# Kernel tuning notes

Hardware: AMD Instinct MI355X
Metric: run time of the kernel (lower is better)

## Reference

```python
import jax, jax.numpy as jnp
import numpy as np
import math

P = 7          # patch / kernel size (must be odd for onion-peeling: N = 1+4*m*(m+1) = P*P)
EPS = 1e-6
EPS_W = 0.5

def _ball_dirs():
    u = [np.array([[1.0, 0.0]])]
    s = [np.zeros(1)]
    for k in range(1, P // 2 + 1):
        n = 8 * k
        th = np.linspace(0.0, 2.0 * math.pi * (1.0 - 1.0 / n), n)
        u.append(np.stack([np.cos(th), np.sin(th)], 1))
        s.append(np.full(n, k / (P // 2)))
    return (np.concatenate(u, 0).astype(np.float32), np.concatenate(s).astype(np.float32))

_U, _S = _ball_dirs()  # [N,2], [N], N == P*P == 49

def _forward(x, metric_w, metric_b, proj_w, proj_b):
    B, C, H, W = x.shape
    Hp, Wp = H // P, W // P
    u = jnp.asarray(_U)
    s = jnp.asarray(_S)
    # metric net: strided conv -> 7 params per patch
    params = jax.lax.conv_general_dilated(
        x, metric_w, (P, P), 'VALID',
        dimension_numbers=('NCHW', 'OIHW', 'NCHW')) + metric_b[None, :, None, None]
    v_raw = jnp.moveaxis(params[:, :2], 1, -1)                      # [B,Hp,Wp,2]
    v = v_raw / jnp.maximum(jnp.linalg.norm(v_raw, axis=-1, keepdims=True), 1e-12)
    eig = 2.0 * jax.nn.sigmoid(jnp.moveaxis(params[:, 2:4], 1, -1))  # [B,Hp,Wp,2]
    scale = 0.5 + 1.5 * jax.nn.sigmoid(jnp.moveaxis(params[:, 4:5], 1, -1))
    eig = eig * scale
    vp = jnp.stack([-v[..., 1], v[..., 0]], -1)
    R = jnp.stack([v, vp], -1)                                      # [B,Hp,Wp,2,2] (columns v, v_perp)
    M = R @ (eig[..., None] * jnp.swapaxes(R, -1, -2))              # R diag(eig) R^T
    w = params[:, 5:7]                                              # [B,2,Hp,Wp]
    w = w * (1.0 - EPS_W) * jax.nn.sigmoid(jnp.linalg.norm(w, axis=1, keepdims=True))
    # Finsler-Randers norm F(u) = sqrt(u^T M u + eps) + w.u for all N unit dirs
    quad = jnp.einsum('nj,bhwij,ni->bnhw', u, M, u)                 # [B,N,Hp,Wp]
    drift = jnp.einsum('bihw,ni->bnhw', w, u)
    F_u = jnp.sqrt(quad + EPS) + drift
    y = (u[None, :, :, None, None] / (F_u[:, :, None] + EPS)
         * s[None, :, None, None, None])                            # [B,N,2,Hp,Wp]
    y = y.reshape(B, P, P, 2, Hp, Wp)[:, :, :, ::-1]                # flip last coord pair (x,y)->(y,x)
    gi = jnp.arange(P, dtype=x.dtype) - P // 2
    grid = jnp.stack(jnp.meshgrid(gi, gi, indexing='ij'), -1)       # [P,P,2]
    off = y - grid[None, :, :, :, None, None]                       # [B,P,P,2,Hp,Wp]
    off_y = jnp.transpose(off[:, :, :, 0], (0, 3, 4, 1, 2))         # [B,Hp,Wp,P,P]
    off_x = jnp.transpose(off[:, :, :, 1], (0, 3, 4, 1, 2))
    base_h = (jnp.arange(Hp, dtype=x.dtype) * P)[None, :, None, None, None]
    base_w = (jnp.arange(Wp, dtype=x.dtype) * P)[None, None, :, None, None]
    ki = jnp.arange(P, dtype=x.dtype)
    py = off_y + base_h + ki[None, None, None, :, None]             # sample rows
    px = off_x + base_w + ki[None, None, None, None, :]             # sample cols
    # bilinear sampling with zero padding (torchvision deform_conv2d semantics)
    y0 = jnp.floor(py)
    x0 = jnp.floor(px)
    wy = py - y0
    wx = px - x0

    def gather(yi, xi):
        valid = (yi >= 0) & (yi <= H - 1) & (xi >= 0) & (xi <= W - 1)
        yc = jnp.clip(yi, 0, H - 1).astype(jnp.int32)
        xc = jnp.clip(xi, 0, W - 1).astype(jnp.int32)
        vals = jax.vmap(lambda img, yy, xx: img[:, yy, xx])(x, yc, xc)  # [B,C,Hp,Wp,P,P]
        return vals * valid[:, None].astype(x.dtype)

    sampled = (gather(y0, x0) * ((1 - wy) * (1 - wx))[:, None]
               + gather(y0, x0 + 1) * ((1 - wy) * wx)[:, None]
               + gather(y0 + 1, x0) * (wy * (1 - wx))[:, None]
               + gather(y0 + 1, x0 + 1) * (wy * wx)[:, None])       # [B,C,Hp,Wp,P,P]
    out = jnp.einsum('bchwij,ecij->behw', sampled, proj_w) + proj_b[None, :, None, None]
    return jnp.moveaxis(out.reshape(B, out.shape[1], -1), 1, 2)     # [B, Hp*Wp, E]

def setup_inputs():
    key = jax.random.key(0)
    k0, k1, k2 = jax.random.split(key, 3)
    B, C, H, W, E = 64, 3, 224, 224, 384
    x = jax.random.normal(k0, (B, C, H, W), jnp.float32)
    metric_w = jax.random.normal(k1, (7, C, P, P), jnp.float32) / math.sqrt(C * P * P)
    metric_b = jnp.zeros((7,), jnp.float32)
    proj_w = jax.random.normal(k2, (E, C, P, P), jnp.float32) / (P * math.sqrt(C))
    proj_b = jnp.zeros((E,), jnp.float32)
    return {"x": x, "metric_w": metric_w, "metric_b": metric_b,
            "proj_w": proj_w, "proj_b": proj_b}

def reference(x, metric_w, metric_b, proj_w, proj_b):
    return _forward(x, metric_w, metric_b, proj_w, proj_b)
```

## Files before the change

kernel.cpp:

```cpp
#include <hip/hip_runtime.h>
#include <math.h>

#define PP   7
#define NDIR 49
#define CIN  3
#define KK   147
#define KPAD 160
#define EE   384
#define HH   224
#define WW   224
#define GG   16
#define TB   256
#define SSTR 17
#define NPX  112

typedef __attribute__((ext_vector_type(8))) __bf16 bf16x8;
typedef __attribute__((ext_vector_type(4))) float  f32x4;

__device__ __forceinline__ float sigmoidf_(float v) {
    return 1.0f / (1.0f + expf(-v));
}

__global__ void pack_pw_kernel(const float* __restrict__ pw, unsigned short* __restrict__ pwB) {
    int idx = blockIdx.x * blockDim.x + threadIdx.x;
    if (idx < EE * KPAD) {
        int e = idx / KPAD;
        int k = idx - e * KPAD;
        float v = (k < KK) ? pw[e * KK + k] : 0.0f;
        __bf16 h = (__bf16)v;
        pwB[idx] = *(unsigned short*)&h;
    }
}

__global__ void pack_x_kernel(const float* __restrict__ x, float* __restrict__ xp, int npix) {
    int idx = blockIdx.x * blockDim.x + threadIdx.x;
    if (idx >= npix) return;
    int b = idx / (HH * WW);
    int p = idx - b * (HH * WW);
    const float* xb = x + (size_t)b * (CIN * HH * WW) + p;
    f32x4 v;
    v[0] = xb[0];
    v[1] = xb[HH * WW];
    v[2] = xb[2 * HH * WW];
    v[3] = 0.0f;
    *(f32x4*)(xp + (size_t)idx * 4) = v;
}

template<bool PACKED>
__launch_bounds__(TB)
__global__ void fused_kernel(const float* __restrict__ x,
                             const float* __restrict__ xp,
                             const float* __restrict__ mw,
                             const float* __restrict__ mb,
                             const unsigned short* __restrict__ pwB,
                             const float* __restrict__ pb,
                             float* __restrict__ out) {
    __shared__ float mws[7 * KK];
    __shared__ float dirs[NDIR][3];
    __shared__ float par_s[GG][8];
    __shared__ float der_s[GG][5];
    __shared__ float buf[3136];

    const int t   = threadIdx.x;
    const int blk = blockIdx.x;
    const int b   = blk >> 6;
    const int rem = blk & 63;
    const int hp  = rem >> 1;
    const int wp0 = (rem & 1) * GG;
    const size_t m0 = (size_t)blk * GG;
    const int row0 = hp * PP;
    const int col0 = wp0 * PP;

    for (int i = t; i < 7 * KK; i += TB) mws[i] = mw[i];
    if (t >= 64 && t < 64 + NDIR) {
        int n = t - 64;
        float u0, u1, s;
        if (n == 0)      { u0 = 1.0f; u1 = 0.0f; s = 0.0f; }
        else if (n < 9)  { float th = (float)(n - 1)  * 0.78539816339744831f; u0 = cosf(th); u1 = sinf(th); s = 0.33333334f; }
        else if (n < 25) { float th = (float)(n - 9)  * 0.39269908169872414f; u0 = cosf(th); u1 = sinf(th); s = 0.66666669f; }
        else             { float th = (float)(n - 25) * 0.26179938779914941f; u0 = cosf(th); u1 = sinf(th); s = 1.0f; }
        dirs[n][0] = u0; dirs[n][1] = u1; dirs[n][2] = s;
    }

    if (PACKED) {
        for (int item = t; item < 7 * NPX; item += TB) {
            int i = item / NPX, px = item - i * NPX;
            f32x4 v = *(const f32x4*)(xp + ((size_t)((b * HH + row0 + i) * WW) + col0 + px) * 4);
            *(f32x4*)&buf[item * 4] = v;
        }
    } else {
        for (int item = t; item < CIN * 7 * NPX; item += TB) {
            int c = item / (7 * NPX), r2 = item - c * (7 * NPX);
            int i = r2 / NPX, px = r2 - i * NPX;
            buf[item] = x[(size_t)b * (CIN * HH * WW) + (size_t)c * (HH * WW)
                          + (size_t)(row0 + i) * WW + col0 + px];
        }
    }
    __syncthreads();

    if (t < 112) {
        int prm = t >> 4, g = t & 15;
        float acc = mb[prm];
        const float* wrow = &mws[prm * KK];
        #pragma unroll
        for (int c = 0; c < CIN; ++c) {
            #pragma unroll
            for (int i = 0; i < 7; ++i) {
                #pragma unroll
                for (int j = 0; j < 7; ++j) {
                    float xv = PACKED ? buf[(i * NPX + g * 7 + j) * 4 + c]
                                      : buf[(c * 7 + i) * NPX + g * 7 + j];
                    acc = fmaf(xv, wrow[c * 49 + i * 7 + j], acc);
                }
            }
        }
        par_s[g][prm] = acc;
    }
    __syncthreads();

    if (t < GG) {
        float a0 = par_s[t][0], a1 = par_s[t][1], a2 = par_s[t][2], a3 = par_s[t][3];
        float a4 = par_s[t][4], a5 = par_s[t][5], a6 = par_s[t][6];
        float nrm = sqrtf(a0 * a0 + a1 * a1);
        float inv = 1.0f / fmaxf(nrm, 1e-12f);
        float v0 = a0 * inv, v1 = a1 * inv;
        float e0 = 2.0f * sigmoidf_(a2);
        float e1 = 2.0f * sigmoidf_(a3);
        float sc = 0.5f + 1.5f * sigmoidf_(a4);
        e0 *= sc; e1 *= sc;
        float wn  = sqrtf(a5 * a5 + a6 * a6);
        float wsc = 0.5f * sigmoidf_(wn);
        der_s[t][0] = e0 * v0 * v0 + e1 * v1 * v1;
        der_s[t][1] = (e0 - e1) * v0 * v1;
        der_s[t][2] = e0 * v1 * v1 + e1 * v0 * v0;
        der_s[t][3] = a5 * wsc;
        der_s[t][4] = a6 * wsc;
    }
    __syncthreads();

    const float* xb = x + (size_t)b * (CIN * HH * WW);
    const size_t pbase = (size_t)b * (HH * WW);
    for (int item = t; item < GG * NDIR; item += TB) {
        int g = item / NDIR;
        int n = item - g * NDIR;
        float u0 = dirs[n][0], u1 = dirs[n][1], s = dirs[n][2];
        float M00 = der_s[g][0], M01 = der_s[g][1], M11 = der_s[g][2];
        float w0 = der_s[g][3], w1 = der_s[g][4];
        float quad  = u0 * u0 * M00 + 2.0f * u0 * u1 * M01 + u1 * u1 * M11;
        float drift = w0 * u0 + w1 * u1;
        float F = sqrtf(quad + 1e-6f) + drift;
        float r = s / (F + 1e-6f);
        float py = (float)(row0 + 3) + u1 * r;
        float px = (float)(col0 + g * PP + 3) + u0 * r;
        float y0f = floorf(py), x0f = floorf(px);
        float y1f = y0f + 1.0f, x1f = x0f + 1.0f;
        float wy = py - y0f, wx = px - x0f;
        bool vy0 = (y0f >= 0.0f) && (y0f <= (float)(HH - 1));
        bool vy1 = (y1f >= 0.0f) && (y1f <= (float)(HH - 1));
        bool vx0 = (x0f >= 0.0f) && (x0f <= (float)(WW - 1));
        bool vx1 = (x1f >= 0.0f) && (x1f <= (float)(WW - 1));
        int iy0 = (int)fminf(fmaxf(y0f, 0.0f), (float)(HH - 1));
        int iy1 = (int)fminf(fmaxf(y1f, 0.0f), (float)(HH - 1));
        int ix0 = (int)fminf(fmaxf(x0f, 0.0f), (float)(WW - 1));
        int ix1 = (int)fminf(fmaxf(x1f, 0.0f), (float)(WW - 1));
        float w00 = (1.0f - wy) * (1.0f - wx);
        float w01 = (1.0f - wy) * wx;
        float w10 = wy * (1.0f - wx);
        float w11 = wy * wx;
        if (PACKED) {
            float c00 = w00 * ((vy0 && vx0) ? 1.0f : 0.0f);
            float c01 = w01 * ((vy0 && vx1) ? 1.0f : 0.0f);
            float c10 = w10 * ((vy1 && vx0) ? 1.0f : 0.0f);
            float c11 = w11 * ((vy1 && vx1) ? 1.0f : 0.0f);
            f32x4 q00 = *(const f32x4*)(xp + (pbase + (size_t)(iy0 * WW + ix0)) * 4);
            f32x4 q01 = *(const f32x4*)(xp + (pbase + (size_t)(iy0 * WW + ix1)) * 4);
            f32x4 q10 = *(const f32x4*)(xp + (pbase + (size_t)(iy1 * WW + ix0)) * 4);
            f32x4 q11 = *(const f32x4*)(xp + (pbase + (size_t)(iy1 * WW + ix1)) * 4);
            #pragma unroll
            for (int c = 0; c < CIN; ++c) {
                buf[(c * NDIR + n) * SSTR + g] =
                    q00[c] * c00 + q01[c] * c01 + q10[c] * c10 + q11[c] * c11;
            }
        } else {
            #pragma unroll
            for (int c = 0; c < CIN; ++c) {
                const float* xc = xb + c * (HH * WW);
                float v00 = (vy0 && vx0) ? xc[iy0 * WW + ix0] : 0.0f;
                float v01 = (vy0 && vx1) ? xc[iy0 * WW + ix1] : 0.0f;
                float v10 = (vy1 && vx0) ? xc[iy1 * WW + ix0] : 0.0f;
                float v11 = (vy1 && vx1) ? xc[iy1 * WW + ix1] : 0.0f;
                buf[(c * NDIR + n) * SSTR + g] =
                    v00 * w00 + v01 * w01 + v10 * w10 + v11 * w11;
            }
        }
    }
    __syncthreads();

    const int lane = t & 63;
    const int wv   = t >> 6;
    const int nrow = lane & 15;
    const int hi   = lane >> 4;

    bf16x8 afr[5];
    #pragma unroll
    for (int ks = 0; ks < 5; ++ks) {
        #pragma unroll
        for (int j = 0; j < 8; ++j) {
            int k = ks * 32 + hi * 8 + j;
            float v = (k < KK) ? buf[k * SSTR + nrow] : 0.0f;
            afr[ks][j] = (__bf16)v;
        }
    }

    #pragma unroll
    for (int q = 0; q < 6; ++q) {
        int tile = wv * 6 + q;
        int e    = tile * 16 + nrow;
        const unsigned short* brow = pwB + (size_t)e * KPAD + hi * 8;
        f32x4 acc = {0.0f, 0.0f, 0.0f, 0.0f};
        #pragma unroll
        for (int ks = 0; ks < 5; ++ks) {
            bf16x8 bfr = *(const bf16x8*)&brow[ks * 32];
            acc = __builtin_amdgcn_mfma_f32_16x16x32_bf16(afr[ks], bfr, acc, 0, 0, 0);
        }
        float bias = pb[e];
        #pragma unroll
        for (int r = 0; r < 4; ++r) {
            out[(m0 + hi * 4 + r) * EE + e] = acc[r] + bias;
        }
    }
}

extern "C" void kernel_launch(void* const* d_in, const int* in_sizes, int n_in,
                              void* d_out, int out_size, void* d_ws, size_t ws_size,
                              hipStream_t stream) {
    const float* x  = (const float*)d_in[0];
    const float* mw = (const float*)d_in[1];
    const float* mb = (const float*)d_in[2];
    const float* pw = (const float*)d_in[3];
    const float* pb = (const float*)d_in[4];
    float* out = (float*)d_out;

    unsigned short* pwB = (unsigned short*)d_ws;
    float* xp = (float*)((char*)d_ws + (size_t)(1 << 17));

    const int B = in_sizes[0] / (CIN * HH * WW);
    const int npix = B * HH * WW;
    const size_t need = (size_t)(1 << 17) + (size_t)npix * 4 * sizeof(float);
    const bool packed = ws_size >= need;

    pack_pw_kernel<<<(EE * KPAD + 255) / 256, 256, 0, stream>>>(pw, pwB);
    if (packed) {
        pack_x_kernel<<<(npix + 255) / 256, 256, 0, stream>>>(x, xp, npix);
        fused_kernel<true><<<B * 64, TB, 0, stream>>>(x, xp, mw, mb, pwB, pb, out);
    } else {
        fused_kernel<false><<<B * 64, TB, 0, stream>>>(x, xp, mw, mb, pwB, pb, out);
    }
}
```

Baseline: 235.7 us.

## Drop packed-x pre-pass, gather from planar input, transpose MFMA for vector stores

Removes the pack_x pre-kernel and its interleaved RGBA workspace, so every block reads the planar input directly for both the metric conv tile and the bilinear gather. This cuts the shared buffer size and adds a launch bound of 6 blocks per CU for occupancy. The gather now loads unconditionally from clamped indices and masks the weights instead of the loads. The MFMA operands are swapped so each lane holds four consecutive output channels, allowing float4 bias loads and float4 output stores. The risk is less coalesced gather traffic on the planar layout, which now takes three scalar loads per corner instead of one vector load.

```diff
diff --git a/kernel.cpp b/kernel.cpp
--- a/kernel.cpp
+++ b/kernel.cpp
@@ -32,24 +32,8 @@
     }
 }
 
-__global__ void pack_x_kernel(const float* __restrict__ x, float* __restrict__ xp, int npix) {
-    int idx = blockIdx.x * blockDim.x + threadIdx.x;
-    if (idx >= npix) return;
-    int b = idx / (HH * WW);
-    int p = idx - b * (HH * WW);
-    const float* xb = x + (size_t)b * (CIN * HH * WW) + p;
-    f32x4 v;
-    v[0] = xb[0];
-    v[1] = xb[HH * WW];
-    v[2] = xb[2 * HH * WW];
-    v[3] = 0.0f;
-    *(f32x4*)(xp + (size_t)idx * 4) = v;
-}
-
-template<bool PACKED>
-__launch_bounds__(TB)
+__launch_bounds__(TB, 6)
 __global__ void fused_kernel(const float* __restrict__ x,
-                             const float* __restrict__ xp,
                              const float* __restrict__ mw,
                              const float* __restrict__ mb,
                              const unsigned short* __restrict__ pwB,
@@ -59,7 +43,7 @@
     __shared__ float dirs[NDIR][3];
     __shared__ float par_s[GG][8];
     __shared__ float der_s[GG][5];
-    __shared__ float buf[3136];
+    __shared__ __align__(16) float buf[2512];
 
     const int t   = threadIdx.x;
     const int blk = blockIdx.x;
@@ -71,6 +55,8 @@
     const int row0 = hp * PP;
     const int col0 = wp0 * PP;
 
+    const float* xb = x + (size_t)b * (CIN * HH * WW);
+
     for (int i = t; i < 7 * KK; i += TB) mws[i] = mw[i];
     if (t >= 64 && t < 64 + NDIR) {
         int n = t - 64;
@@ -82,39 +68,33 @@
         dirs[n][0] = u0; dirs[n][1] = u1; dirs[n][2] = s;
     }
 
-    if (PACKED) {
-        for (int item = t; item < 7 * NPX; item += TB) {
-            int i = item / NPX, px = item - i * NPX;
-            f32x4 v = *(const f32x4*)(xp + ((size_t)((b * HH + row0 + i) * WW) + col0 + px) * 4);
-            *(f32x4*)&buf[item * 4] = v;
-        }
-    } else {
-        for (int item = t; item < CIN * 7 * NPX; item += TB) {
-            int c = item / (7 * NPX), r2 = item - c * (7 * NPX);
-            int i = r2 / NPX, px = r2 - i * NPX;
-            buf[item] = x[(size_t)b * (CIN * HH * WW) + (size_t)c * (HH * WW)
-                          + (size_t)(row0 + i) * WW + col0 + px];
-        }
+    for (int item = t; item < CIN * 7 * NPX; item += TB) {
+        int c = item / (7 * NPX), r2 = item - c * (7 * NPX);
+        int i = r2 / NPX, px = r2 - i * NPX;
+        buf[item] = xb[(size_t)c * (HH * WW) + (size_t)(row0 + i) * WW + col0 + px];
     }
     __syncthreads();
 
     if (t < 112) {
         int prm = t >> 4, g = t & 15;
-        float acc = mb[prm];
         const float* wrow = &mws[prm * KK];
-        #pragma unroll
-        for (int c = 0; c < CIN; ++c) {
+        float acc0 = 0.0f, acc1 = 0.0f, acc2 = 0.0f;
+        #pragma unroll 1
+        for (int i = 0; i < 7; ++i) {
+            const float* b0 = &buf[(0 * 7 + i) * NPX + g * 7];
+            const float* b1 = &buf[(1 * 7 + i) * NPX + g * 7];
+            const float* b2 = &buf[(2 * 7 + i) * NPX + g * 7];
+            const float* w0 = &wrow[i * 7];
+            const float* w1 = &wrow[49 + i * 7];
+            const float* w2 = &wrow[98 + i * 7];
             #pragma unroll
-            for (int i = 0; i < 7; ++i) {
-                #pragma unroll
-                for (int j = 0; j < 7; ++j) {
-                    float xv = PACKED ? buf[(i * NPX + g * 7 + j) * 4 + c]
-                                      : buf[(c * 7 + i) * NPX + g * 7 + j];
-                    acc = fmaf(xv, wrow[c * 49 + i * 7 + j], acc);
-                }
+            for (int j = 0; j < 7; ++j) {
+                acc0 = fmaf(b0[j], w0[j], acc0);
+                acc1 = fmaf(b1[j], w1[j], acc1);
+                acc2 = fmaf(b2[j], w2[j], acc2);
             }
         }
-        par_s[g][prm] = acc;
+        par_s[g][prm] = mb[prm] + acc0 + acc1 + acc2;
     }
     __syncthreads();
 
@@ -138,59 +118,48 @@
     }
     __syncthreads();
 
-    const float* xb = x + (size_t)b * (CIN * HH * WW);
-    const size_t pbase = (size_t)b * (HH * WW);
-    for (int item = t; item < GG * NDIR; item += TB) {
-        int g = item / NDIR;
-        int n = item - g * NDIR;
-        float u0 = dirs[n][0], u1 = dirs[n][1], s = dirs[n][2];
-        float M00 = der_s[g][0], M01 = der_s[g][1], M11 = der_s[g][2];
-        float w0 = der_s[g][3], w1 = der_s[g][4];
-        float quad  = u0 * u0 * M00 + 2.0f * u0 * u1 * M01 + u1 * u1 * M11;
-        float drift = w0 * u0 + w1 * u1;
-        float F = sqrtf(quad + 1e-6f) + drift;
-        float r = s / (F + 1e-6f);
-        float py = (float)(row0 + 3) + u1 * r;
-        float px = (float)(col0 + g * PP + 3) + u0 * r;
-        float y0f = floorf(py), x0f = floorf(px);
-        float y1f = y0f + 1.0f, x1f = x0f + 1.0f;
-        float wy = py - y0f, wx = px - x0f;
-        bool vy0 = (y0f >= 0.0f) && (y0f <= (float)(HH - 1));
-        bool vy1 = (y1f >= 0.0f) && (y1f <= (float)(HH - 1));
-        bool vx0 = (x0f >= 0.0f) && (x0f <= (float)(WW - 1));
-        bool vx1 = (x1f >= 0.0f) && (x1f <= (float)(WW - 1));
-        int iy0 = (int)fminf(fmaxf(y0f, 0.0f), (float)(HH - 1));
-        int iy1 = (int)fminf(fmaxf(y1f, 0.0f), (float)(HH - 1));
-        int ix0 = (int)fminf(fmaxf(x0f, 0.0f), (float)(WW - 1));
-        int ix1 = (int)fminf(fmaxf(x1f, 0.0f), (float)(WW - 1));
-        float w00 = (1.0f - wy) * (1.0f - wx);
-        float w01 = (1.0f - wy) * wx;
-        float w10 = wy * (1.0f - wx);
-        float w11 = wy * wx;
-        if (PACKED) {
-            float c00 = w00 * ((vy0 && vx0) ? 1.0f : 0.0f);
-            float c01 = w01 * ((vy0 && vx1) ? 1.0f : 0.0f);
-            float c10 = w10 * ((vy1 && vx0) ? 1.0f : 0.0f);
-            float c11 = w11 * ((vy1 && vx1) ? 1.0f : 0.0f);
-            f32x4 q00 = *(const f32x4*)(xp + (pbase + (size_t)(iy0 * WW + ix0)) * 4);
-            f32x4 q01 = *(const f32x4*)(xp + (pbase + (size_t)(iy0 * WW + ix1)) * 4);
-            f32x4 q10 = *(const f32x4*)(xp + (pbase + (size_t)(iy1 * WW + ix0)) * 4);
-            f32x4 q11 = *(const f32x4*)(xp + (pbase + (size_t)(iy1 * WW + ix1)) * 4);
-            #pragma unroll
-            for (int c = 0; c < CIN; ++c) {
-                buf[(c * NDIR + n) * SSTR + g] =
-                    q00[c] * c00 + q01[c] * c01 + q10[c] * c10 + q11[c] * c11;
-            }
-        } else {
+    #pragma unroll
+    for (int rep = 0; rep < 4; ++rep) {
+        int item = rep * TB + t;
+        if (item < GG * NDIR) {
+            int g = item / NDIR;
+            int n = item - g * NDIR;
+            float u0 = dirs[n][0], u1 = dirs[n][1], s = dirs[n][2];
+            float M00 = der_s[g][0], M01 = der_s[g][1], M11 = der_s[g][2];
+            float w0 = der_s[g][3], w1 = der_s[g][4];
+            float quad  = u0 * u0 * M00 + 2.0f * u0 * u1 * M01 + u1 * u1 * M11;
+            float drift = w0 * u0 + w1 * u1;
+            float F = sqrtf(quad + 1e-6f) + drift;
+            float r = s / (F + 1e-6f);
+            float py = (float)(row0 + 3) + u1 * r;
+            float px = (float)(col0 + g * PP + 3) + u0 * r;
+            float y0f = floorf(py), x0f = floorf(px);
+            float y1f = y0f + 1.0f, x1f = x0f + 1.0f;
+            float wy = py - y0f, wx = px - x0f;
+            float c00 = (1.0f - wy) * (1.0f - wx);
+            float c01 = (1.0f - wy) * wx;
+            float c10 = wy * (1.0f - wx);
+            float c11 = wy * wx;
+            bool vy0 = (y0f >= 0.0f) && (y0f <= (float)(HH - 1));
+            bool vy1 = (y1f >= 0.0f) && (y1f <= (float)(HH - 1));
+            bool vx0 = (x0f >= 0.0f) && (x0f <= (float)(WW - 1));
+            bool vx1 = (x1f >= 0.0f) && (x1f <= (float)(WW - 1));
+            c00 *= (vy0 && vx0) ? 1.0f : 0.0f;
+            c01 *= (vy0 && vx1) ? 1.0f : 0.0f;
+            c10 *= (vy1 && vx0) ? 1.0f : 0.0f;
+            c11 *= (vy1 && vx1) ? 1.0f : 0.0f;
+            int iy0 = (int)fminf(fmaxf(y0f, 0.0f), (float)(HH - 1));
+            int iy1 = (int)fminf(fmaxf(y1f, 0.0f), (float)(HH - 1));
+            int ix0 = (int)fminf(fmaxf(x0f, 0.0f), (float)(WW - 1));
+            int ix1 = (int)fminf(fmaxf(x1f, 0.0f), (float)(WW - 1));
+            int o00 = iy0 * WW + ix0, o01 = iy0 * WW + ix1;
+            int o10 = iy1 * WW + ix0, o11 = iy1 * WW + ix1;
             #pragma unroll
             for (int c = 0; c < CIN; ++c) {
                 const float* xc = xb + c * (HH * WW);
-                float v00 = (vy0 && vx0) ? xc[iy0 * WW + ix0] : 0.0f;
-                float v01 = (vy0 && vx1) ? xc[iy0 * WW + ix1] : 0.0f;
-                float v10 = (vy1 && vx0) ? xc[iy1 * WW + ix0] : 0.0f;
-                float v11 = (vy1 && vx1) ? xc[iy1 * WW + ix1] : 0.0f;
+                float v00 = xc[o00], v01 = xc[o01], v10 = xc[o10], v11 = xc[o11];
                 buf[(c * NDIR + n) * SSTR + g] =
-                    v00 * w00 + v01 * w01 + v10 * w10 + v11 * w11;
+                    v00 * c00 + v01 * c01 + v10 * c10 + v11 * c11;
             }
         }
     }
@@ -201,33 +170,33 @@
     const int nrow = lane & 15;
     const int hi   = lane >> 4;
 
-    bf16x8 afr[5];
+    bf16x8 sfr[5];
     #pragma unroll
     for (int ks = 0; ks < 5; ++ks) {
         #pragma unroll
         for (int j = 0; j < 8; ++j) {
             int k = ks * 32 + hi * 8 + j;
             float v = (k < KK) ? buf[k * SSTR + nrow] : 0.0f;
-            afr[ks][j] = (__bf16)v;
-        }
-    }
-
+            sfr[ks][j] = (__bf16)v;
+        }
+    }
+
+    float* orow = out + (m0 + nrow) * EE;
     #pragma unroll
     for (int q = 0; q < 6; ++q) {
         int tile = wv * 6 + q;
-        int e    = tile * 16 + nrow;
-        const unsigned short* brow = pwB + (size_t)e * KPAD + hi * 8;
+        int erow = tile * 16 + nrow;
+        const unsigned short* arow = pwB + (size_t)erow * KPAD + hi * 8;
         f32x4 acc = {0.0f, 0.0f, 0.0f, 0.0f};
         #pragma unroll
         for (int ks = 0; ks < 5; ++ks) {
-            bf16x8 bfr = *(const bf16x8*)&brow[ks * 32];
-            acc = __builtin_amdgcn_mfma_f32_16x16x32_bf16(afr[ks], bfr, acc, 0, 0, 0);
-        }
-        float bias = pb[e];
-        #pragma unroll
-        for (int r = 0; r < 4; ++r) {
-            out[(m0 + hi * 4 + r) * EE + e] = acc[r] + bias;
-        }
+            bf16x8 afr = *(const bf16x8*)&arow[ks * 32];
+            acc = __builtin_amdgcn_mfma_f32_16x16x32_bf16(afr, sfr[ks], acc, 0, 0, 0);
+        }
+        int e0 = tile * 16 + hi * 4;
+        f32x4 b4 = *(const f32x4*)&pb[e0];
+        f32x4 o = acc + b4;
+        *(f32x4*)&orow[e0] = o;
     }
 }
 
@@ -242,18 +211,9 @@
     float* out = (float*)d_out;
 
     unsigned short* pwB = (unsigned short*)d_ws;
-    float* xp = (float*)((char*)d_ws + (size_t)(1 << 17));
 
     const int B = in_sizes[0] / (CIN * HH * WW);
-    const int npix = B * HH * WW;
-    const size_t need = (size_t)(1 << 17) + (size_t)npix * 4 * sizeof(float);
-    const bool packed = ws_size >= need;
 
     pack_pw_kernel<<<(EE * KPAD + 255) / 256, 256, 0, stream>>>(pw, pwB);
-    if (packed) {
-        pack_x_kernel<<<(npix + 255) / 256, 256, 0, stream>>>(x, xp, npix);
-        fused_kernel<true><<<B * 64, TB, 0, stream>>>(x, xp, mw, mb, pwB, pb, out);
-    } else {
-        fused_kernel<false><<<B * 64, TB, 0, stream>>>(x, xp, mw, mb, pwB, pb, out);
-    }
-}
+    fused_kernel<<<B * 64, TB, 0, stream>>>(x, mw, mb, pwB, pb, out);
+}
```

Result: faster. 214.9 us (-8.8%).
